# Kernel optimization log

Measured on AMD Instinct MI355X. Metric: run time of the kernel, lower is better.

The kernel has to match this reference:

```python
import jax, jax.numpy as jnp
import numpy as np

N = 100000
E = 1600000
IN_C = 128
OUT_C = 32
BN_EPS = 1e-5


def setup_inputs() -> dict:
    key = jax.random.key(0)
    k1, k2, k3, k4, k5, k6 = jax.random.split(key, 6)
    x = jax.random.normal(k1, (N, IN_C), dtype=jnp.float32)
    edge_index = jax.random.randint(k2, (2, E), 0, N, dtype=jnp.int64)
    # GCNConv linear weight (glorot-ish) and bias
    W = jax.random.normal(k3, (IN_C, OUT_C), dtype=jnp.float32) / np.sqrt(IN_C)
    b = jax.random.normal(k4, (OUT_C,), dtype=jnp.float32) * 0.01
    # BatchNorm1d affine params
    gamma = jnp.ones((OUT_C,), dtype=jnp.float32) + 0.1 * jax.random.normal(k5, (OUT_C,), dtype=jnp.float32)
    beta = 0.1 * jax.random.normal(k6, (OUT_C,), dtype=jnp.float32)
    return {"x": x, "edge_index": edge_index, "W": W, "b": b, "gamma": gamma, "beta": beta}


def reference(x, edge_index, W, b, gamma, beta):
    # --- GCNConv (PyG semantics): add self-loops, sym degree norm, linear ---
    self_loops = jnp.arange(N, dtype=edge_index.dtype)
    row = jnp.concatenate([edge_index[0], self_loops])  # source nodes [E+N]
    col = jnp.concatenate([edge_index[1], self_loops])  # target nodes [E+N]

    deg = jax.ops.segment_sum(jnp.ones_like(col, dtype=x.dtype), col, num_segments=N)
    deg_inv_sqrt = jnp.where(deg > 0, jax.lax.rsqrt(deg), 0.0)
    norm = deg_inv_sqrt[row] * deg_inv_sqrt[col]  # [E+N]

    h = x @ W  # project first (PyG order): [N, OUT_C]
    msgs = norm[:, None] * h[row]  # gather + scale: [E+N, OUT_C]
    out = jax.ops.segment_sum(msgs, col, num_segments=N) + b  # scatter-add

    # --- BatchNorm1d (training mode: batch statistics, biased variance) ---
    mean = jnp.mean(out, axis=0)
    var = jnp.mean((out - mean) ** 2, axis=0)
    y = (out - mean) * jax.lax.rsqrt(var + BN_EPS) * gamma + beta
    return y
```

## Files before the change

kernel.cpp:

```cpp
#include <hip/hip_runtime.h>
#include <hip/hip_fp16.h>

#define IN_C  128
#define OUT_C 32
#define BN_EPS 1e-5f
#define BKT_BITS 7
#define BKT 128
#define C_CAP 2816
#define CH  6144

__global__ void zero_kernel(int* __restrict__ bcnt, float* __restrict__ sums) {
    int i = threadIdx.x;
    if (i < 1024) bcnt[i] = 0;
    if (i < 512) sums[i] = 0.0f;
}

__global__ __launch_bounds__(512) void binfill_kernel(
    const int* __restrict__ row, const int* __restrict__ col,
    int* __restrict__ bcnt, int* __restrict__ adjp, int E)
{
    __shared__ int pk[CH];
    __shared__ unsigned short bk[CH];
    __shared__ int h[1024];
    __shared__ int excl[1024];
    __shared__ int lcur[1024];
    __shared__ int basg[1024];
    __shared__ int sc[512];
    const int t  = threadIdx.x;
    const int e0 = blockIdx.x * CH;
    const int n  = min(CH, E - e0);

    for (int i = t; i < 1024; i += 512) h[i] = 0;
    __syncthreads();

    int myb[12], myp[12];
    #pragma unroll
    for (int k = 0; k < 12; ++k) {
        int i = t + 512 * k;
        myb[k] = -1;
        if (i < n) {
            int c = col[e0 + i];
            int r = row[e0 + i];
            myb[k] = c >> BKT_BITS;
            myp[k] = (r << BKT_BITS) | (c & (BKT - 1));
            atomicAdd(&h[myb[k]], 1);
        }
    }
    __syncthreads();

    int a  = h[2 * t];
    int b2 = h[2 * t + 1];
    int s = a + b2;
    sc[t] = s; __syncthreads();
    for (int off = 1; off < 512; off <<= 1) {
        int u = (t >= off) ? sc[t - off] : 0;
        __syncthreads();
        sc[t] += u;
        __syncthreads();
    }
    {
        int pre = sc[t] - s;
        excl[2 * t] = pre;          lcur[2 * t] = pre;
        excl[2 * t + 1] = pre + a;  lcur[2 * t + 1] = pre + a;
        int g0 = 0, g1 = 0;
        if (a)  { g0 = atomicAdd(&bcnt[2 * t], a);      if (g0 > C_CAP - a)  g0 = max(0, C_CAP - a); }
        if (b2) { g1 = atomicAdd(&bcnt[2 * t + 1], b2); if (g1 > C_CAP - b2) g1 = max(0, C_CAP - b2); }
        basg[2 * t]     = (2 * t) * C_CAP + g0;
        basg[2 * t + 1] = (2 * t + 1) * C_CAP + g1;
    }
    __syncthreads();

    #pragma unroll
    for (int k = 0; k < 12; ++k) {
        if (myb[k] >= 0) {
            int b = myb[k];
            int l = atomicAdd(&lcur[b], 1);
            pk[l] = myp[k];
            bk[l] = (unsigned short)b;
        }
    }
    __syncthreads();

    for (int i = t; i < n; i += 512) {
        int b = bk[i];
        adjp[basg[b] + (i - excl[b])] = pk[i];
    }
}

__global__ __launch_bounds__(256) void sort_kernel(
    const int* __restrict__ bcnt, int* __restrict__ adjp,
    int* __restrict__ offs, int* __restrict__ counts, int N)
{
    __shared__ int eL[C_CAP];
    __shared__ int h[BKT];
    __shared__ int cur[BKT];
    __shared__ int sc[BKT];
    const int t = threadIdx.x;
    const int b = blockIdx.x;
    const int s0  = b * C_CAP;
    const int cnt = min(bcnt[b], C_CAP);

    if (t < BKT) h[t] = 0;
    __syncthreads();
    for (int i = t; i < cnt; i += 256) {
        int p = adjp[s0 + i];
        eL[i] = p;
        atomicAdd(&h[p & (BKT - 1)], 1);
    }
    __syncthreads();

    if (t < BKT) sc[t] = h[t];
    __syncthreads();
    for (int off = 1; off < BKT; off <<= 1) {
        int u = (t >= off && t < BKT) ? sc[t - off] : 0;
        __syncthreads();
        if (t < BKT) sc[t] += u;
        __syncthreads();
    }
    if (t < BKT) {
        int e = sc[t] - h[t];
        cur[t] = e;
        int nd = (b << BKT_BITS) + t;
        if (nd < N) { offs[nd] = s0 + e; counts[nd] = h[t]; }
    }
    __syncthreads();

    for (int i = t; i < cnt; i += 256) {
        int p = eL[i];
        int pos = atomicAdd(&cur[p & (BKT - 1)], 1);
        adjp[s0 + pos] = p >> BKT_BITS;
    }
}

__global__ __launch_bounds__(256) void gemm_kernel(
    const float* __restrict__ x, const float* __restrict__ W,
    const int* __restrict__ counts, __half* __restrict__ gh0,
    __half* __restrict__ gh1, int N)
{
    __shared__ float xs[32 * 132];
    __shared__ float wl[128 * 32];
    const int tid = threadIdx.x;
    const int r0  = blockIdx.x * 32;

    #pragma unroll
    for (int k = 0; k < 4; ++k) {
        int idx = tid + 256 * k;
        int row = idx >> 5;
        int c4  = idx & 31;
        int rr  = r0 + row;
        float4 v = make_float4(0.f, 0.f, 0.f, 0.f);
        if (rr < N) v = reinterpret_cast<const float4*>(x)[(size_t)rr * 32 + c4];
        *reinterpret_cast<float4*>(&xs[row * 132 + c4 * 4]) = v;
    }
    #pragma unroll
    for (int k = 0; k < 4; ++k) {
        int idx = tid + 256 * k;
        reinterpret_cast<float4*>(wl)[idx] = reinterpret_cast<const float4*>(W)[idx];
    }
    __syncthreads();

    const int r_local = tid >> 3;
    const int c4 = (tid & 7) * 4;
    float4 sum = make_float4(0.f, 0.f, 0.f, 0.f);
    #pragma unroll 8
    for (int k = 0; k < 128; ++k) {
        float  xv = xs[r_local * 132 + k];
        float4 w4 = *reinterpret_cast<const float4*>(&wl[k * 32 + c4]);
        sum.x = fmaf(xv, w4.x, sum.x);
        sum.y = fmaf(xv, w4.y, sum.y);
        sum.z = fmaf(xv, w4.z, sum.z);
        sum.w = fmaf(xv, w4.w, sum.w);
    }
    const int r = r0 + r_local;
    if (r < N) {
        float dis = rsqrtf((float)counts[r] + 1.0f);
        union { __half2 h[2]; float2 f; } u;
        u.h[0] = __floats2half2_rn(sum.x * dis, sum.y * dis);
        u.h[1] = __floats2half2_rn(sum.z * dis, sum.w * dis);
        __half* tb = (c4 < 16) ? gh0 : gh1;
        reinterpret_cast<float2*>(tb)[(size_t)r * 4 + ((c4 & 15) >> 2)] = u.f;
    }
}

__global__ __launch_bounds__(256) void pull_kernel(
    const int* __restrict__ counts, const int* __restrict__ offs,
    const int* __restrict__ adj2, const __half* __restrict__ gh0,
    const __half* __restrict__ gh1, const float* __restrict__ bias,
    float* __restrict__ out, float* __restrict__ sums, int N, int PB)
{
    const int xcd  = blockIdx.x & 7;
    const int half = xcd >> 2;
    const int idx  = (blockIdx.x >> 3) * 4 + (xcd & 3);

    __shared__ float4 r1[256];
    __shared__ float4 r2[256];
    const int t   = threadIdx.x;
    const int grp = t >> 4;
    const int way = (t >> 2) & 3;
    const int l4  = t & 3;
    const int chan_off = half * 16;
    const float2* g2 = reinterpret_cast<const float2*>(half ? gh1 : gh0);
    const float4 bc = *reinterpret_cast<const float4*>(&bias[chan_off + l4 * 4]);

    float4 ls = make_float4(0.f, 0.f, 0.f, 0.f);
    float4 lq = make_float4(0.f, 0.f, 0.f, 0.f);

    const int n0 = idx * 32 + grp * 2;
    const int n1 = n0 + 1;
    if (idx < PB && n0 < N) {
        const int start = offs[n0];
        const int len0  = counts[n0];
        const int len1  = (n1 < N) ? counts[n1] : 0;
        const int total = len0 + len1;

        float a00 = 0.f, a01 = 0.f, a02 = 0.f, a03 = 0.f;
        float a10 = 0.f, a11 = 0.f, a12 = 0.f, a13 = 0.f;
        if (way == 0) {
            float2 raw = g2[(size_t)n0 * 4 + l4];
            __half2 p = *reinterpret_cast<__half2*>(&raw.x);
            __half2 q = *reinterpret_cast<__half2*>(&raw.y);
            float2 xx = __half22float2(p), yy = __half22float2(q);
            a00 = xx.x; a01 = xx.y; a02 = yy.x; a03 = yy.y;
        } else if (way == 1 && n1 < N) {
            float2 raw = g2[(size_t)n1 * 4 + l4];
            __half2 p = *reinterpret_cast<__half2*>(&raw.x);
            __half2 q = *reinterpret_cast<__half2*>(&raw.y);
            float2 xx = __half22float2(p), yy = __half22float2(q);
            a10 = xx.x; a11 = xx.y; a12 = yy.x; a13 = yy.y;
        }

        #define ACC2(w, s) { \
            __half2 p = *reinterpret_cast<__half2*>(&(w).x); \
            __half2 q = *reinterpret_cast<__half2*>(&(w).y); \
            float2 xx = __half22float2(p), yy = __half22float2(q); \
            a00 += (s) ? xx.x : 0.f;  a10 += (s) ? 0.f : xx.x; \
            a01 += (s) ? xx.y : 0.f;  a11 += (s) ? 0.f : xx.y; \
            a02 += (s) ? yy.x : 0.f;  a12 += (s) ? 0.f : yy.x; \
            a03 += (s) ? yy.y : 0.f;  a13 += (s) ? 0.f : yy.y; }

        int k = way;
        for (; k + 28 < total; k += 32) {
            int e0 = adj2[start + k];
            int e1 = adj2[start + k + 4];
            int e2 = adj2[start + k + 8];
            int e3 = adj2[start + k + 12];
            int e4 = adj2[start + k + 16];
            int e5 = adj2[start + k + 20];
            int e6 = adj2[start + k + 24];
            int e7 = adj2[start + k + 28];
            float2 w0 = g2[(size_t)e0 * 4 + l4];
            float2 w1 = g2[(size_t)e1 * 4 + l4];
            float2 w2 = g2[(size_t)e2 * 4 + l4];
            float2 w3 = g2[(size_t)e3 * 4 + l4];
            float2 w4 = g2[(size_t)e4 * 4 + l4];
            float2 w5 = g2[(size_t)e5 * 4 + l4];
            float2 w6 = g2[(size_t)e6 * 4 + l4];
            float2 w7 = g2[(size_t)e7 * 4 + l4];
            ACC2(w0, k      < len0) ACC2(w1, k + 4  < len0)
            ACC2(w2, k + 8  < len0) ACC2(w3, k + 12 < len0)
            ACC2(w4, k + 16 < len0) ACC2(w5, k + 20 < len0)
            ACC2(w6, k + 24 < len0) ACC2(w7, k + 28 < len0)
        }
        for (; k + 12 < total; k += 16) {
            int e0 = adj2[start + k];
            int e1 = adj2[start + k + 4];
            int e2 = adj2[start + k + 8];
            int e3 = adj2[start + k + 12];
            float2 w0 = g2[(size_t)e0 * 4 + l4];
            float2 w1 = g2[(size_t)e1 * 4 + l4];
            float2 w2 = g2[(size_t)e2 * 4 + l4];
            float2 w3 = g2[(size_t)e3 * 4 + l4];
            ACC2(w0, k      < len0) ACC2(w1, k + 4  < len0)
            ACC2(w2, k + 8  < len0) ACC2(w3, k + 12 < len0)
        }
        for (; k < total; k += 4) {
            int e0 = adj2[start + k];
            float2 w0 = g2[(size_t)e0 * 4 + l4];
            ACC2(w0, k < len0)
        }
        #undef ACC2

        a00 += __shfl_xor(a00, 4); a00 += __shfl_xor(a00, 8);
        a01 += __shfl_xor(a01, 4); a01 += __shfl_xor(a01, 8);
        a02 += __shfl_xor(a02, 4); a02 += __shfl_xor(a02, 8);
        a03 += __shfl_xor(a03, 4); a03 += __shfl_xor(a03, 8);
        a10 += __shfl_xor(a10, 4); a10 += __shfl_xor(a10, 8);
        a11 += __shfl_xor(a11, 4); a11 += __shfl_xor(a11, 8);
        a12 += __shfl_xor(a12, 4); a12 += __shfl_xor(a12, 8);
        a13 += __shfl_xor(a13, 4); a13 += __shfl_xor(a13, 8);

        if (way == 0) {
            float dis = rsqrtf((float)len0 + 1.0f);
            float4 v;
            v.x = fmaf(dis, a00, bc.x);
            v.y = fmaf(dis, a01, bc.y);
            v.z = fmaf(dis, a02, bc.z);
            v.w = fmaf(dis, a03, bc.w);
            reinterpret_cast<float4*>(out)[(size_t)n0 * 8 + (chan_off >> 2) + l4] = v;
            ls.x += v.x; ls.y += v.y; ls.z += v.z; ls.w += v.w;
            lq.x = fmaf(v.x, v.x, lq.x); lq.y = fmaf(v.y, v.y, lq.y);
            lq.z = fmaf(v.z, v.z, lq.z); lq.w = fmaf(v.w, v.w, lq.w);
        } else if (way == 1 && n1 < N) {
            float dis = rsqrtf((float)len1 + 1.0f);
            float4 v;
            v.x = fmaf(dis, a10, bc.x);
            v.y = fmaf(dis, a11, bc.y);
            v.z = fmaf(dis, a12, bc.z);
            v.w = fmaf(dis, a13, bc.w);
            reinterpret_cast<float4*>(out)[(size_t)n1 * 8 + (chan_off >> 2) + l4] = v;
            ls.x += v.x; ls.y += v.y; ls.z += v.z; ls.w += v.w;
            lq.x = fmaf(v.x, v.x, lq.x); lq.y = fmaf(v.y, v.y, lq.y);
            lq.z = fmaf(v.z, v.z, lq.z); lq.w = fmaf(v.w, v.w, lq.w);
        }
    }

    r1[t] = ls; r2[t] = lq;
    __syncthreads();
    #pragma unroll
    for (int off = 128; off >= 4; off >>= 1) {
        if (t < off) {
            float4 u1 = r1[t + off], u2 = r2[t + off];
            float4 v1 = r1[t],       v2 = r2[t];
            v1.x += u1.x; v1.y += u1.y; v1.z += u1.z; v1.w += u1.w;
            v2.x += u2.x; v2.y += u2.y; v2.z += u2.z; v2.w += u2.w;
            r1[t] = v1; r2[t] = v2;
        }
        __syncthreads();
    }
    if (t < 4) {
        float4 v1 = r1[t], v2 = r2[t];
        float* sb = sums + (blockIdx.x & 7) * 64;
        int cb = chan_off + 4 * t;
        atomicAdd(&sb[cb + 0], v1.x); atomicAdd(&sb[cb + 1], v1.y);
        atomicAdd(&sb[cb + 2], v1.z); atomicAdd(&sb[cb + 3], v1.w);
        atomicAdd(&sb[32 + cb + 0], v2.x); atomicAdd(&sb[32 + cb + 1], v2.y);
        atomicAdd(&sb[32 + cb + 2], v2.z); atomicAdd(&sb[32 + cb + 3], v2.w);
    }
}

__global__ void stats_kernel(const float* __restrict__ sums,
                             const float* __restrict__ gamma,
                             const float* __restrict__ beta,
                             float* __restrict__ ss, int N)
{
    int c = threadIdx.x;
    if (c < 32) {
        float s = 0.f, q = 0.f;
        #pragma unroll
        for (int r = 0; r < 8; ++r) { s += sums[r * 64 + c]; q += sums[r * 64 + 32 + c]; }
        float invN  = 1.0f / (float)N;
        float mean  = s * invN;
        float var   = q * invN - mean * mean;
        float scale = gamma[c] * rsqrtf(var + BN_EPS);
        ss[c]      = scale;
        ss[32 + c] = fmaf(-mean, scale, beta[c]);
    }
}

__global__ __launch_bounds__(256) void bn_apply_kernel(
    float* __restrict__ out, const float* __restrict__ ss, long long n4)
{
    long long i = (long long)blockIdx.x * blockDim.x + threadIdx.x;
    if (i < n4) {
        int c4 = (int)(i & 7) * 4;
        float4 v = reinterpret_cast<float4*>(out)[i];
        v.x = fmaf(v.x, ss[c4 + 0], ss[32 + c4 + 0]);
        v.y = fmaf(v.y, ss[c4 + 1], ss[32 + c4 + 1]);
        v.z = fmaf(v.z, ss[c4 + 2], ss[32 + c4 + 2]);
        v.w = fmaf(v.w, ss[c4 + 3], ss[32 + c4 + 3]);
        reinterpret_cast<float4*>(out)[i] = v;
    }
}

extern "C" void kernel_launch(void* const* d_in, const int* in_sizes, int n_in,
                              void* d_out, int out_size, void* d_ws, size_t ws_size,
                              hipStream_t stream)
{
    const float* x     = (const float*)d_in[0];
    const int*   ei    = (const int*)d_in[1];
    const float* W     = (const float*)d_in[2];
    const float* b     = (const float*)d_in[3];
    const float* gamma = (const float*)d_in[4];
    const float* beta  = (const float*)d_in[5];
    float* out = (float*)d_out;

    const int N = in_sizes[0] / IN_C;
    const int E = in_sizes[1] / 2;
    const int* row = ei;
    const int* col = ei + E;
    const int NB = (N + BKT - 1) >> BKT_BITS;

    __half* gh0   = (__half*)d_ws;
    __half* gh1   = gh0 + (size_t)N * 16;
    float* sums   = (float*)(gh1 + (size_t)N * 16);
    float* ss     = sums + 512;
    int*   counts = (int*)(sums + 576);
    int*   offs   = counts + N;
    int*   bcnt   = offs + N;
    int*   adjp   = bcnt + 1024;

    zero_kernel   <<<1, 1024, 0, stream>>>(bcnt, sums);
    binfill_kernel<<<(E + CH - 1) / CH, 512, 0, stream>>>(row, col, bcnt, adjp, E);
    sort_kernel   <<<NB, 256, 0, stream>>>(bcnt, adjp, offs, counts, N);

    gemm_kernel   <<<(N + 31) / 32, 256, 0, stream>>>(x, W, counts, gh0, gh1, N);

    const int PB   = (N + 31) / 32;
    const int grid = ((PB + 3) / 4) * 8;
    pull_kernel   <<<grid, 256, 0, stream>>>(counts, offs, adjp, gh0, gh1, b, out, sums, N, PB);

    stats_kernel  <<<1, 64, 0, stream>>>(sums, gamma, beta, ss, N);

    long long n4 = (long long)N * OUT_C / 4;
    bn_apply_kernel<<<(int)((n4 + 255) / 256), 256, 0, stream>>>(out, ss, n4);
}
```

Measured before the change: 127.2 us.

## Degree-sort nodes within buckets and assign one node per 16-thread group in pull

The sort kernel now builds a per-bucket permutation of nodes ordered by in-degree, written to a new order array, and pads unused slots with -1. The pull kernel processes one node per 16-thread group taken from that order, replacing the previous two-nodes-per-group scheme with its per-edge select masks. This is meant to cut wavefront divergence from uneven degrees and drop the dual-accumulator select overhead. The cost is an extra scan in the sort kernel, an extra indirection load, and twice as many pull blocks.

```diff
diff --git a/kernel.cpp b/kernel.cpp
--- a/kernel.cpp
+++ b/kernel.cpp
@@ -89,18 +89,22 @@
 
 __global__ __launch_bounds__(256) void sort_kernel(
     const int* __restrict__ bcnt, int* __restrict__ adjp,
-    int* __restrict__ offs, int* __restrict__ counts, int N)
+    int* __restrict__ offs, int* __restrict__ counts,
+    int* __restrict__ order, int N)
 {
     __shared__ int eL[C_CAP];
     __shared__ int h[BKT];
     __shared__ int cur[BKT];
     __shared__ int sc[BKT];
+    __shared__ int dh[BKT];
+    __shared__ int dcur[BKT];
     const int t = threadIdx.x;
     const int b = blockIdx.x;
     const int s0  = b * C_CAP;
     const int cnt = min(bcnt[b], C_CAP);
-
-    if (t < BKT) h[t] = 0;
+    const int base = b << BKT_BITS;
+
+    if (t < BKT) { h[t] = 0; dh[t] = 0; }
     __syncthreads();
     for (int i = t; i < cnt; i += 256) {
         int p = adjp[s0 + i];
@@ -117,11 +121,36 @@
         if (t < BKT) sc[t] += u;
         __syncthreads();
     }
+    int valid = 0, mydeg = 0;
     if (t < BKT) {
         int e = sc[t] - h[t];
         cur[t] = e;
-        int nd = (b << BKT_BITS) + t;
-        if (nd < N) { offs[nd] = s0 + e; counts[nd] = h[t]; }
+        int nd = base + t;
+        if (nd < N) {
+            offs[nd] = s0 + e; counts[nd] = h[t];
+            valid = 1; mydeg = min(h[t], BKT - 1);
+            atomicAdd(&dh[mydeg], 1);
+        }
+    }
+    __syncthreads();
+
+    if (t < BKT) sc[t] = dh[t];
+    __syncthreads();
+    for (int off = 1; off < BKT; off <<= 1) {
+        int u = (t >= off && t < BKT) ? sc[t - off] : 0;
+        __syncthreads();
+        if (t < BKT) sc[t] += u;
+        __syncthreads();
+    }
+    if (t < BKT) dcur[t] = sc[t] - dh[t];
+    __syncthreads();
+    if (t < BKT) {
+        if (valid) {
+            int r = atomicAdd(&dcur[mydeg], 1);
+            order[base + r] = base + t;
+        }
+        int nvalid = min(N - base, BKT);
+        if (t >= nvalid) order[base + t] = -1;
     }
     __syncthreads();
 
@@ -184,9 +213,10 @@
 
 __global__ __launch_bounds__(256) void pull_kernel(
     const int* __restrict__ counts, const int* __restrict__ offs,
-    const int* __restrict__ adj2, const __half* __restrict__ gh0,
-    const __half* __restrict__ gh1, const float* __restrict__ bias,
-    float* __restrict__ out, float* __restrict__ sums, int N, int PB)
+    const int* __restrict__ adj2, const int* __restrict__ order,
+    const __half* __restrict__ gh0, const __half* __restrict__ gh1,
+    const float* __restrict__ bias, float* __restrict__ out,
+    float* __restrict__ sums, int PB)
 {
     const int xcd  = blockIdx.x & 7;
     const int half = xcd >> 2;
@@ -205,41 +235,29 @@
     float4 ls = make_float4(0.f, 0.f, 0.f, 0.f);
     float4 lq = make_float4(0.f, 0.f, 0.f, 0.f);
 
-    const int n0 = idx * 32 + grp * 2;
-    const int n1 = n0 + 1;
-    if (idx < PB && n0 < N) {
-        const int start = offs[n0];
-        const int len0  = counts[n0];
-        const int len1  = (n1 < N) ? counts[n1] : 0;
-        const int total = len0 + len1;
-
-        float a00 = 0.f, a01 = 0.f, a02 = 0.f, a03 = 0.f;
-        float a10 = 0.f, a11 = 0.f, a12 = 0.f, a13 = 0.f;
+    int nd = -1;
+    if (idx < PB) nd = order[idx * 16 + grp];
+    if (nd >= 0) {
+        const int start = offs[nd];
+        const int len   = counts[nd];
+
+        float a0 = 0.f, a1 = 0.f, a2 = 0.f, a3 = 0.f;
         if (way == 0) {
-            float2 raw = g2[(size_t)n0 * 4 + l4];
+            float2 raw = g2[(size_t)nd * 4 + l4];
             __half2 p = *reinterpret_cast<__half2*>(&raw.x);
             __half2 q = *reinterpret_cast<__half2*>(&raw.y);
             float2 xx = __half22float2(p), yy = __half22float2(q);
-            a00 = xx.x; a01 = xx.y; a02 = yy.x; a03 = yy.y;
-        } else if (way == 1 && n1 < N) {
-            float2 raw = g2[(size_t)n1 * 4 + l4];
-            __half2 p = *reinterpret_cast<__half2*>(&raw.x);
-            __half2 q = *reinterpret_cast<__half2*>(&raw.y);
-            float2 xx = __half22float2(p), yy = __half22float2(q);
-            a10 = xx.x; a11 = xx.y; a12 = yy.x; a13 = yy.y;
-        }
-
-        #define ACC2(w, s) { \
+            a0 = xx.x; a1 = xx.y; a2 = yy.x; a3 = yy.y;
+        }
+
+        #define ACC(w) { \
             __half2 p = *reinterpret_cast<__half2*>(&(w).x); \
             __half2 q = *reinterpret_cast<__half2*>(&(w).y); \
             float2 xx = __half22float2(p), yy = __half22float2(q); \
-            a00 += (s) ? xx.x : 0.f;  a10 += (s) ? 0.f : xx.x; \
-            a01 += (s) ? xx.y : 0.f;  a11 += (s) ? 0.f : xx.y; \
-            a02 += (s) ? yy.x : 0.f;  a12 += (s) ? 0.f : yy.x; \
-            a03 += (s) ? yy.y : 0.f;  a13 += (s) ? 0.f : yy.y; }
+            a0 += xx.x; a1 += xx.y; a2 += yy.x; a3 += yy.y; }
 
         int k = way;
-        for (; k + 28 < total; k += 32) {
+        for (; k + 28 < len; k += 32) {
             int e0 = adj2[start + k];
             int e1 = adj2[start + k + 4];
             int e2 = adj2[start + k + 8];
@@ -256,12 +274,9 @@
             float2 w5 = g2[(size_t)e5 * 4 + l4];
             float2 w6 = g2[(size_t)e6 * 4 + l4];
             float2 w7 = g2[(size_t)e7 * 4 + l4];
-            ACC2(w0, k      < len0) ACC2(w1, k + 4  < len0)
-            ACC2(w2, k + 8  < len0) ACC2(w3, k + 12 < len0)
-            ACC2(w4, k + 16 < len0) ACC2(w5, k + 20 < len0)
-            ACC2(w6, k + 24 < len0) ACC2(w7, k + 28 < len0)
-        }
-        for (; k + 12 < total; k += 16) {
+            ACC(w0) ACC(w1) ACC(w2) ACC(w3) ACC(w4) ACC(w5) ACC(w6) ACC(w7)
+        }
+        for (; k + 12 < len; k += 16) {
             int e0 = adj2[start + k];
             int e1 = adj2[start + k + 4];
             int e2 = adj2[start + k + 8];
@@ -270,44 +285,28 @@
             float2 w1 = g2[(size_t)e1 * 4 + l4];
             float2 w2 = g2[(size_t)e2 * 4 + l4];
             float2 w3 = g2[(size_t)e3 * 4 + l4];
-            ACC2(w0, k      < len0) ACC2(w1, k + 4  < len0)
-            ACC2(w2, k + 8  < len0) ACC2(w3, k + 12 < len0)
-        }
-        for (; k < total; k += 4) {
+            ACC(w0) ACC(w1) ACC(w2) ACC(w3)
+        }
+        for (; k < len; k += 4) {
             int e0 = adj2[start + k];
             float2 w0 = g2[(size_t)e0 * 4 + l4];
-            ACC2(w0, k < len0)
-        }
-        #undef ACC2
-
-        a00 += __shfl_xor(a00, 4); a00 += __shfl_xor(a00, 8);
-        a01 += __shfl_xor(a01, 4); a01 += __shfl_xor(a01, 8);
-        a02 += __shfl_xor(a02, 4); a02 += __shfl_xor(a02, 8);
-        a03 += __shfl_xor(a03, 4); a03 += __shfl_xor(a03, 8);
-        a10 += __shfl_xor(a10, 4); a10 += __shfl_xor(a10, 8);
-        a11 += __shfl_xor(a11, 4); a11 += __shfl_xor(a11, 8);
-        a12 += __shfl_xor(a12, 4); a12 += __shfl_xor(a12, 8);
-        a13 += __shfl_xor(a13, 4); a13 += __shfl_xor(a13, 8);
+            ACC(w0)
+        }
+        #undef ACC
+
+        a0 += __shfl_xor(a0, 4); a0 += __shfl_xor(a0, 8);
+        a1 += __shfl_xor(a1, 4); a1 += __shfl_xor(a1, 8);
+        a2 += __shfl_xor(a2, 4); a2 += __shfl_xor(a2, 8);
+        a3 += __shfl_xor(a3, 4); a3 += __shfl_xor(a3, 8);
 
         if (way == 0) {
-            float dis = rsqrtf((float)len0 + 1.0f);
+            float dis = rsqrtf((float)len + 1.0f);
             float4 v;
-            v.x = fmaf(dis, a00, bc.x);
-            v.y = fmaf(dis, a01, bc.y);
-            v.z = fmaf(dis, a02, bc.z);
-            v.w = fmaf(dis, a03, bc.w);
-            reinterpret_cast<float4*>(out)[(size_t)n0 * 8 + (chan_off >> 2) + l4] = v;
-            ls.x += v.x; ls.y += v.y; ls.z += v.z; ls.w += v.w;
-            lq.x = fmaf(v.x, v.x, lq.x); lq.y = fmaf(v.y, v.y, lq.y);
-            lq.z = fmaf(v.z, v.z, lq.z); lq.w = fmaf(v.w, v.w, lq.w);
-        } else if (way == 1 && n1 < N) {
-            float dis = rsqrtf((float)len1 + 1.0f);
-            float4 v;
-            v.x = fmaf(dis, a10, bc.x);
-            v.y = fmaf(dis, a11, bc.y);
-            v.z = fmaf(dis, a12, bc.z);
-            v.w = fmaf(dis, a13, bc.w);
-            reinterpret_cast<float4*>(out)[(size_t)n1 * 8 + (chan_off >> 2) + l4] = v;
+            v.x = fmaf(dis, a0, bc.x);
+            v.y = fmaf(dis, a1, bc.y);
+            v.z = fmaf(dis, a2, bc.z);
+            v.w = fmaf(dis, a3, bc.w);
+            reinterpret_cast<float4*>(out)[(size_t)nd * 8 + (chan_off >> 2) + l4] = v;
             ls.x += v.x; ls.y += v.y; ls.z += v.z; ls.w += v.w;
             lq.x = fmaf(v.x, v.x, lq.x); lq.y = fmaf(v.y, v.y, lq.y);
             lq.z = fmaf(v.z, v.z, lq.z); lq.w = fmaf(v.w, v.w, lq.w);
@@ -397,17 +396,18 @@
     int*   counts = (int*)(sums + 576);
     int*   offs   = counts + N;
     int*   bcnt   = offs + N;
-    int*   adjp   = bcnt + 1024;
+    int*   order  = bcnt + 1024;
+    int*   adjp   = order + (size_t)NB * BKT;
 
     zero_kernel   <<<1, 1024, 0, stream>>>(bcnt, sums);
     binfill_kernel<<<(E + CH - 1) / CH, 512, 0, stream>>>(row, col, bcnt, adjp, E);
-    sort_kernel   <<<NB, 256, 0, stream>>>(bcnt, adjp, offs, counts, N);
+    sort_kernel   <<<NB, 256, 0, stream>>>(bcnt, adjp, offs, counts, order, N);
 
     gemm_kernel   <<<(N + 31) / 32, 256, 0, stream>>>(x, W, counts, gh0, gh1, N);
 
-    const int PB   = (N + 31) / 32;
+    const int PB   = NB * 8;
     const int grid = ((PB + 3) / 4) * 8;
-    pull_kernel   <<<grid, 256, 0, stream>>>(counts, offs, adjp, gh0, gh1, b, out, sums, N, PB);
+    pull_kernel   <<<grid, 256, 0, stream>>>(counts, offs, adjp, order, gh0, gh1, b, out, sums, PB);
 
     stats_kernel  <<<1, 64, 0, stream>>>(sums, gamma, beta, ss, N);
 
```

Measured after the change: 164.9 us. 1.3x slower.

## Pair nodes by degree rank for load balancing and fuse BN stats into apply

Applied to the files above, without the earlier changes.

The sort kernel now ranks the nodes within each 32-node group by in-degree and writes a permutation. The pull kernel pairs the lowest-degree node with the highest-degree node in each 16-lane group so that neighbour-loop lengths within a wavefront are more uniform, which reduces divergence and idle lanes. Edge-index loads and output stores use nontemporal hints. The stats kernel is folded into bn_apply, with every block recomputing the 32-channel scale and shift, which removes one launch at the cost of redundant small reads per block.

```diff
diff --git a/kernel.cpp b/kernel.cpp
--- a/kernel.cpp
+++ b/kernel.cpp
@@ -8,6 +8,8 @@
 #define BKT 128
 #define C_CAP 2816
 #define CH  6144
+
+typedef float floatx4 __attribute__((ext_vector_type(4)));
 
 __global__ void zero_kernel(int* __restrict__ bcnt, float* __restrict__ sums) {
     int i = threadIdx.x;
@@ -89,16 +91,19 @@
 
 __global__ __launch_bounds__(256) void sort_kernel(
     const int* __restrict__ bcnt, int* __restrict__ adjp,
-    int* __restrict__ offs, int* __restrict__ counts, int N)
+    int* __restrict__ offs, int* __restrict__ counts,
+    int* __restrict__ order, int N)
 {
     __shared__ int eL[C_CAP];
     __shared__ int h[BKT];
     __shared__ int cur[BKT];
     __shared__ int sc[BKT];
+    __shared__ int wdeg[BKT];
     const int t = threadIdx.x;
     const int b = blockIdx.x;
     const int s0  = b * C_CAP;
     const int cnt = min(bcnt[b], C_CAP);
+    const int base = b << BKT_BITS;
 
     if (t < BKT) h[t] = 0;
     __syncthreads();
@@ -120,8 +125,22 @@
     if (t < BKT) {
         int e = sc[t] - h[t];
         cur[t] = e;
-        int nd = (b << BKT_BITS) + t;
+        int nd = base + t;
         if (nd < N) { offs[nd] = s0 + e; counts[nd] = h[t]; }
+        wdeg[t] = (nd < N) ? h[t] : -1;
+    }
+    __syncthreads();
+
+    if (t < BKT) {
+        int w0 = t & ~31;
+        int my = wdeg[t];
+        int rank = 0;
+        #pragma unroll
+        for (int j = 0; j < 32; ++j) {
+            int dj = wdeg[w0 + j];
+            rank += (dj < my) || (dj == my && (w0 + j) < t);
+        }
+        order[base + w0 + rank] = (my >= 0) ? (base + t) : -1;
     }
     __syncthreads();
 
@@ -184,9 +203,10 @@
 
 __global__ __launch_bounds__(256) void pull_kernel(
     const int* __restrict__ counts, const int* __restrict__ offs,
-    const int* __restrict__ adj2, const __half* __restrict__ gh0,
-    const __half* __restrict__ gh1, const float* __restrict__ bias,
-    float* __restrict__ out, float* __restrict__ sums, int N, int PB)
+    const int* __restrict__ adj2, const int* __restrict__ order,
+    const __half* __restrict__ gh0, const __half* __restrict__ gh1,
+    const float* __restrict__ bias, float* __restrict__ out,
+    float* __restrict__ sums, int NW)
 {
     const int xcd  = blockIdx.x & 7;
     const int half = xcd >> 2;
@@ -205,23 +225,24 @@
     float4 ls = make_float4(0.f, 0.f, 0.f, 0.f);
     float4 lq = make_float4(0.f, 0.f, 0.f, 0.f);
 
-    const int n0 = idx * 32 + grp * 2;
-    const int n1 = n0 + 1;
-    if (idx < PB && n0 < N) {
-        const int start = offs[n0];
-        const int len0  = counts[n0];
-        const int len1  = (n1 < N) ? counts[n1] : 0;
+    if (idx < NW) {
+        const int n0 = order[idx * 32 + grp];
+        const int n1 = order[idx * 32 + 31 - grp];
+        int s0 = 0, len0 = 0, s1 = 0, len1 = 0;
+        if (n0 >= 0) { s0 = offs[n0]; len0 = counts[n0]; }
+        if (n1 >= 0) { s1 = offs[n1]; len1 = counts[n1]; }
         const int total = len0 + len1;
+        const int s1m = s1 - len0;
 
         float a00 = 0.f, a01 = 0.f, a02 = 0.f, a03 = 0.f;
         float a10 = 0.f, a11 = 0.f, a12 = 0.f, a13 = 0.f;
-        if (way == 0) {
+        if (way == 0 && n0 >= 0) {
             float2 raw = g2[(size_t)n0 * 4 + l4];
             __half2 p = *reinterpret_cast<__half2*>(&raw.x);
             __half2 q = *reinterpret_cast<__half2*>(&raw.y);
             float2 xx = __half22float2(p), yy = __half22float2(q);
             a00 = xx.x; a01 = xx.y; a02 = yy.x; a03 = yy.y;
-        } else if (way == 1 && n1 < N) {
+        } else if (way == 1 && n1 >= 0) {
             float2 raw = g2[(size_t)n1 * 4 + l4];
             __half2 p = *reinterpret_cast<__half2*>(&raw.x);
             __half2 q = *reinterpret_cast<__half2*>(&raw.y);
@@ -229,6 +250,7 @@
             a10 = xx.x; a11 = xx.y; a12 = yy.x; a13 = yy.y;
         }
 
+        #define LDI(kk) __builtin_nontemporal_load(&adj2[(((kk) < len0) ? s0 : s1m) + (kk)])
         #define ACC2(w, s) { \
             __half2 p = *reinterpret_cast<__half2*>(&(w).x); \
             __half2 q = *reinterpret_cast<__half2*>(&(w).y); \
@@ -240,14 +262,14 @@
 
         int k = way;
         for (; k + 28 < total; k += 32) {
-            int e0 = adj2[start + k];
-            int e1 = adj2[start + k + 4];
-            int e2 = adj2[start + k + 8];
-            int e3 = adj2[start + k + 12];
-            int e4 = adj2[start + k + 16];
-            int e5 = adj2[start + k + 20];
-            int e6 = adj2[start + k + 24];
-            int e7 = adj2[start + k + 28];
+            int e0 = LDI(k);
+            int e1 = LDI(k + 4);
+            int e2 = LDI(k + 8);
+            int e3 = LDI(k + 12);
+            int e4 = LDI(k + 16);
+            int e5 = LDI(k + 20);
+            int e6 = LDI(k + 24);
+            int e7 = LDI(k + 28);
             float2 w0 = g2[(size_t)e0 * 4 + l4];
             float2 w1 = g2[(size_t)e1 * 4 + l4];
             float2 w2 = g2[(size_t)e2 * 4 + l4];
@@ -262,10 +284,10 @@
             ACC2(w6, k + 24 < len0) ACC2(w7, k + 28 < len0)
         }
         for (; k + 12 < total; k += 16) {
-            int e0 = adj2[start + k];
-            int e1 = adj2[start + k + 4];
-            int e2 = adj2[start + k + 8];
-            int e3 = adj2[start + k + 12];
+            int e0 = LDI(k);
+            int e1 = LDI(k + 4);
+            int e2 = LDI(k + 8);
+            int e3 = LDI(k + 12);
             float2 w0 = g2[(size_t)e0 * 4 + l4];
             float2 w1 = g2[(size_t)e1 * 4 + l4];
             float2 w2 = g2[(size_t)e2 * 4 + l4];
@@ -274,11 +296,12 @@
             ACC2(w2, k + 8  < len0) ACC2(w3, k + 12 < len0)
         }
         for (; k < total; k += 4) {
-            int e0 = adj2[start + k];
+            int e0 = LDI(k);
             float2 w0 = g2[(size_t)e0 * 4 + l4];
             ACC2(w0, k < len0)
         }
         #undef ACC2
+        #undef LDI
 
         a00 += __shfl_xor(a00, 4); a00 += __shfl_xor(a00, 8);
         a01 += __shfl_xor(a01, 4); a01 += __shfl_xor(a01, 8);
@@ -289,25 +312,25 @@
         a12 += __shfl_xor(a12, 4); a12 += __shfl_xor(a12, 8);
         a13 += __shfl_xor(a13, 4); a13 += __shfl_xor(a13, 8);
 
-        if (way == 0) {
+        if (way == 0 && n0 >= 0) {
             float dis = rsqrtf((float)len0 + 1.0f);
-            float4 v;
+            floatx4 v;
             v.x = fmaf(dis, a00, bc.x);
             v.y = fmaf(dis, a01, bc.y);
             v.z = fmaf(dis, a02, bc.z);
             v.w = fmaf(dis, a03, bc.w);
-            reinterpret_cast<float4*>(out)[(size_t)n0 * 8 + (chan_off >> 2) + l4] = v;
+            __builtin_nontemporal_store(v, &reinterpret_cast<floatx4*>(out)[(size_t)n0 * 8 + (chan_off >> 2) + l4]);
             ls.x += v.x; ls.y += v.y; ls.z += v.z; ls.w += v.w;
             lq.x = fmaf(v.x, v.x, lq.x); lq.y = fmaf(v.y, v.y, lq.y);
             lq.z = fmaf(v.z, v.z, lq.z); lq.w = fmaf(v.w, v.w, lq.w);
-        } else if (way == 1 && n1 < N) {
+        } else if (way == 1 && n1 >= 0) {
             float dis = rsqrtf((float)len1 + 1.0f);
-            float4 v;
+            floatx4 v;
             v.x = fmaf(dis, a10, bc.x);
             v.y = fmaf(dis, a11, bc.y);
             v.z = fmaf(dis, a12, bc.z);
             v.w = fmaf(dis, a13, bc.w);
-            reinterpret_cast<float4*>(out)[(size_t)n1 * 8 + (chan_off >> 2) + l4] = v;
+            __builtin_nontemporal_store(v, &reinterpret_cast<floatx4*>(out)[(size_t)n1 * 8 + (chan_off >> 2) + l4]);
             ls.x += v.x; ls.y += v.y; ls.z += v.z; ls.w += v.w;
             lq.x = fmaf(v.x, v.x, lq.x); lq.y = fmaf(v.y, v.y, lq.y);
             lq.z = fmaf(v.z, v.z, lq.z); lq.w = fmaf(v.w, v.w, lq.w);
@@ -338,36 +361,34 @@
     }
 }
 
-__global__ void stats_kernel(const float* __restrict__ sums,
-                             const float* __restrict__ gamma,
-                             const float* __restrict__ beta,
-                             float* __restrict__ ss, int N)
-{
-    int c = threadIdx.x;
-    if (c < 32) {
+__global__ __launch_bounds__(256) void bn_apply_kernel(
+    float* __restrict__ out, const float* __restrict__ sums,
+    const float* __restrict__ gamma, const float* __restrict__ beta,
+    int N, long long n4)
+{
+    __shared__ float ssl[64];
+    const int t = threadIdx.x;
+    if (t < 32) {
         float s = 0.f, q = 0.f;
         #pragma unroll
-        for (int r = 0; r < 8; ++r) { s += sums[r * 64 + c]; q += sums[r * 64 + 32 + c]; }
+        for (int r = 0; r < 8; ++r) { s += sums[r * 64 + t]; q += sums[r * 64 + 32 + t]; }
         float invN  = 1.0f / (float)N;
         float mean  = s * invN;
         float var   = q * invN - mean * mean;
-        float scale = gamma[c] * rsqrtf(var + BN_EPS);
-        ss[c]      = scale;
-        ss[32 + c] = fmaf(-mean, scale, beta[c]);
-    }
-}
-
-__global__ __launch_bounds__(256) void bn_apply_kernel(
-    float* __restrict__ out, const float* __restrict__ ss, long long n4)
-{
-    long long i = (long long)blockIdx.x * blockDim.x + threadIdx.x;
+        float scale = gamma[t] * rsqrtf(var + BN_EPS);
+        ssl[t]      = scale;
+        ssl[32 + t] = fmaf(-mean, scale, beta[t]);
+    }
+    __syncthreads();
+
+    long long i = (long long)blockIdx.x * blockDim.x + t;
     if (i < n4) {
         int c4 = (int)(i & 7) * 4;
         float4 v = reinterpret_cast<float4*>(out)[i];
-        v.x = fmaf(v.x, ss[c4 + 0], ss[32 + c4 + 0]);
-        v.y = fmaf(v.y, ss[c4 + 1], ss[32 + c4 + 1]);
-        v.z = fmaf(v.z, ss[c4 + 2], ss[32 + c4 + 2]);
-        v.w = fmaf(v.w, ss[c4 + 3], ss[32 + c4 + 3]);
+        v.x = fmaf(v.x, ssl[c4 + 0], ssl[32 + c4 + 0]);
+        v.y = fmaf(v.y, ssl[c4 + 1], ssl[32 + c4 + 1]);
+        v.z = fmaf(v.z, ssl[c4 + 2], ssl[32 + c4 + 2]);
+        v.w = fmaf(v.w, ssl[c4 + 3], ssl[32 + c4 + 3]);
         reinterpret_cast<float4*>(out)[i] = v;
     }
 }
@@ -393,24 +414,22 @@
     __half* gh0   = (__half*)d_ws;
     __half* gh1   = gh0 + (size_t)N * 16;
     float* sums   = (float*)(gh1 + (size_t)N * 16);
-    float* ss     = sums + 512;
     int*   counts = (int*)(sums + 576);
     int*   offs   = counts + N;
     int*   bcnt   = offs + N;
-    int*   adjp   = bcnt + 1024;
+    int*   order  = bcnt + 1024;
+    int*   adjp   = order + (size_t)NB * BKT;
 
     zero_kernel   <<<1, 1024, 0, stream>>>(bcnt, sums);
     binfill_kernel<<<(E + CH - 1) / CH, 512, 0, stream>>>(row, col, bcnt, adjp, E);
-    sort_kernel   <<<NB, 256, 0, stream>>>(bcnt, adjp, offs, counts, N);
+    sort_kernel   <<<NB, 256, 0, stream>>>(bcnt, adjp, offs, counts, order, N);
 
     gemm_kernel   <<<(N + 31) / 32, 256, 0, stream>>>(x, W, counts, gh0, gh1, N);
 
-    const int PB   = (N + 31) / 32;
-    const int grid = ((PB + 3) / 4) * 8;
-    pull_kernel   <<<grid, 256, 0, stream>>>(counts, offs, adjp, gh0, gh1, b, out, sums, N, PB);
-
-    stats_kernel  <<<1, 64, 0, stream>>>(sums, gamma, beta, ss, N);
+    const int NW   = NB * 4;
+    const int grid = ((NW + 3) / 4) * 8;
+    pull_kernel   <<<grid, 256, 0, stream>>>(counts, offs, adjp, order, gh0, gh1, b, out, sums, NW);
 
     long long n4 = (long long)N * OUT_C / 4;
-    bn_apply_kernel<<<(int)((n4 + 255) / 256), 256, 0, stream>>>(out, ss, n4);
-}
+    bn_apply_kernel<<<(int)((n4 + 255) / 256), 256, 0, stream>>>(out, sums, gamma, beta, N, n4);
+}
```

Measured after the change: 128.4 us. About the same (+1.0%).
